# Optimization experiments

Measured on AMD Instinct MI355X. Metric: run time of the kernel, lower is better.

## Reference

```python
import jax, jax.numpy as jnp
import numpy as np

CH = 512
COND = 1280
HEADS = 8
GROUPS = CH // 8
EPS = 1e-5


def conv2d(x, w, b, pad):
    y = jax.lax.conv_general_dilated(
        x, w, window_strides=(1, 1), padding=[(pad, pad), (pad, pad)],
        dimension_numbers=('NCHW', 'OIHW', 'NCHW'))
    return y + b[None, :, None, None]


def group_norm(x, gamma, beta, groups, eps=EPS):
    b, c, h, w = x.shape
    xg = x.reshape(b, groups, c // groups, h, w)
    mu = xg.mean(axis=(2, 3, 4), keepdims=True)
    var = xg.var(axis=(2, 3, 4), keepdims=True)
    xn = ((xg - mu) * jax.lax.rsqrt(var + eps)).reshape(b, c, h, w)
    return xn * gamma[None, :, None, None] + beta[None, :, None, None]


def setup_inputs() -> dict:
    key = jax.random.key(0)
    ks = jax.random.split(key, 20)
    s = 0.05
    inp = {
        'x': jax.random.normal(ks[0], (8, CH, 32, 32), jnp.float32),
        'conditioning': jax.random.normal(ks[1], (8, COND), jnp.float32),
        # ResBlock params
        'c1w': jax.random.normal(ks[2], (CH, CH, 3, 3), jnp.float32) * s,
        'c1b': jnp.zeros((CH,), jnp.float32),
        'g1w': jnp.ones((CH,), jnp.float32),
        'g1b': jnp.zeros((CH,), jnp.float32),
        'c2w': jax.random.normal(ks[3], (CH, CH, 3, 3), jnp.float32) * s,
        'c2b': jnp.zeros((CH,), jnp.float32),
        'g2w': jnp.ones((CH,), jnp.float32),
        'g2b': jnp.zeros((CH,), jnp.float32),
        'cpw': jax.random.normal(ks[4], (CH, COND), jnp.float32) * s,
        'cpb': jnp.zeros((CH,), jnp.float32),
        'rpw': jax.random.normal(ks[5], (CH, CH, 1, 1), jnp.float32) * s,
        'rpb': jnp.zeros((CH,), jnp.float32),
        # Attention params (1x1 convs)
        'qw': jax.random.normal(ks[6], (CH, CH, 1, 1), jnp.float32) * s,
        'qb': jnp.zeros((CH,), jnp.float32),
        'kw': jax.random.normal(ks[7], (CH, CH, 1, 1), jnp.float32) * s,
        'kb': jnp.zeros((CH,), jnp.float32),
        'vw': jax.random.normal(ks[8], (CH, CH, 1, 1), jnp.float32) * s,
        'vb': jnp.zeros((CH,), jnp.float32),
        'ow': jax.random.normal(ks[9], (CH, CH, 1, 1), jnp.float32) * s,
        'ob': jnp.zeros((CH,), jnp.float32),
    }
    return inp


def reference(x, conditioning, c1w, c1b, g1w, g1b, c2w, c2b, g2w, g2b,
              cpw, cpb, rpw, rpb, qw, qb, kw, kb, vw, vb, ow, ob):
    # --- ResBlock ---
    residual = conv2d(x, rpw, rpb, 0)
    h = conv2d(x, c1w, c1b, 1)
    h = group_norm(h, g1w, g1b, GROUPS)
    h = jax.nn.silu(h)
    h = conv2d(h, c2w, c2b, 1)
    h = group_norm(h, g2w, g2b, GROUPS)
    cond = conditioning @ cpw.T + cpb  # [B, C]
    h = h * (1.0 + cond[:, :, None, None]) + residual

    # --- SpatialSelfAttention ---
    b, c, hh, ww = h.shape
    d = c // HEADS
    scale = d ** (-0.5)
    q = conv2d(h, qw, qb, 0).reshape(b, HEADS, d, hh * ww)
    k = conv2d(h, kw, kb, 0).reshape(b, HEADS, d, hh * ww)
    v = conv2d(h, vw, vb, 0).reshape(b, HEADS, d, hh * ww)
    attn = jnp.einsum('bhdn,bhdm->bhnm', q, k) * scale  # [B,H,N,N]
    attn = jax.nn.softmax(attn, axis=-1)
    out = jnp.einsum('bhnm,bhdm->bhdn', attn, v).reshape(b, c, hh, ww)
    return conv2d(out, ow, ob, 0) + h
```

## Files before the change

kernel.cpp:

```cpp
#include <hip/hip_runtime.h>
#include <hip/hip_bf16.h>

typedef unsigned short u16;
typedef __attribute__((ext_vector_type(8))) short bf8;
typedef __attribute__((ext_vector_type(4))) short bf4;
typedef __attribute__((ext_vector_type(4))) float f32x4;

#define CH_ 512
#define NSP 1024
#define NB 8
#define CONDDIM 1280
#define NGROUP 64
#define HEADS_ 8
#define HD 64
#define PR 34
#define PPB (PR*PR)
#define QSCALE 0.18033688011112042f

#define VWAIT(N) asm volatile("s_waitcnt vmcnt(" #N ")" ::: "memory")
#define SCHEDB __builtin_amdgcn_sched_barrier(0)
#define BARRIER do { SCHEDB; __builtin_amdgcn_s_barrier(); SCHEDB; } while (0)

__device__ __forceinline__ u16 f2bf(float f) {
  union { float f; unsigned u; } v; v.f = f;
  unsigned u = v.u;
  return (u16)((u + 0x7fffu + ((u >> 16) & 1u)) >> 16);
}

__device__ __forceinline__ unsigned cvt_pk_bf16(float lo, float hi) {
  unsigned r;
  asm volatile("v_cvt_pk_bf16_f32 %0, %1, %2" : "=v"(r) : "v"(lo), "v"(hi));
  return r;
}

__device__ __forceinline__ f32x4 mfma_bf16(bf8 a, bf8 b, f32x4 c) {
  return __builtin_amdgcn_mfma_f32_16x16x32_bf16(a, b, c, 0, 0, 0);
}

__device__ __forceinline__ void gload16(const void* g, void* l) {
  __builtin_amdgcn_global_load_lds((const __attribute__((address_space(1))) void*)g,
                                   (__attribute__((address_space(3))) void*)l, 16, 0, 0);
}


__global__ __launch_bounds__(1024) void pack_x_kernel(const float* __restrict__ x, u16* __restrict__ xp) {
  __shared__ float t[32][33];
  int b = blockIdx.z;
  int c0 = blockIdx.y * 32, p0 = blockIdx.x * 32;
  int tx = threadIdx.x & 31, ty = threadIdx.x >> 5;
  t[ty][tx] = x[((size_t)b * CH_ + c0 + ty) * NSP + p0 + tx];
  __syncthreads();
  int p = p0 + ty;
  int y = p >> 5, xc = p & 31;
  xp[((size_t)b * PPB + (size_t)(y + 1) * PR + xc + 1) * CH_ + c0 + tx] = f2bf(t[tx][ty]);
}

__global__ __launch_bounds__(256) void border_zero_kernel(u16* __restrict__ a, u16* __restrict__ b) {
  int id = blockIdx.x * 256 + threadIdx.x;
  if (id >= NB * 132 * 64) return;
  int ch8 = id & 63;
  int rest = id >> 6;
  int bidx = rest % 132;
  int bb = rest / 132;
  int r, c;
  if (bidx < 34)       { r = 0;          c = bidx; }
  else if (bidx < 68)  { r = 33;         c = bidx - 34; }
  else if (bidx < 100) { r = bidx - 67;  c = 0; }
  else                 { r = bidx - 99;  c = 33; }
  size_t off = ((size_t)bb * PPB + (size_t)r * PR + c) * CH_ + ch8 * 8;
  const bf8 z = {0, 0, 0, 0, 0, 0, 0, 0};
  *(bf8*)(a + off) = z;
  *(bf8*)(b + off) = z;
}

__global__ __launch_bounds__(256) void pack_w3_kernel(const float* __restrict__ w, u16* __restrict__ wp) {
  int id = blockIdx.x * 256 + threadIdx.x;
  if (id >= 9 * 64 * CH_) return;
  int co = id & (CH_ - 1);
  int cib = (id >> 9) & 63;
  int t = id >> 15;
  int dy = t / 3, dx = t % 3;
  bf8 v;
#pragma unroll
  for (int j = 0; j < 8; j++) {
    int ci = cib * 8 + j;
    v[j] = (short)f2bf(w[(((size_t)co * CH_ + ci) * 3 + dy) * 3 + dx]);
  }
  *(bf8*)(wp + ((size_t)(t * 64 + cib) * CH_ + co) * 8) = v;
}

__global__ __launch_bounds__(256) void pack_w1_kernel(const float* __restrict__ w, u16* __restrict__ wp) {
  int id = blockIdx.x * 256 + threadIdx.x;
  if (id >= 64 * CH_) return;
  int co = id & (CH_ - 1);
  int cib = id >> 9;
  bf8 v;
#pragma unroll
  for (int j = 0; j < 8; j++) v[j] = (short)f2bf(w[(size_t)co * CH_ + cib * 8 + j]);
  *(bf8*)(wp + ((size_t)cib * CH_ + co) * 8) = v;
}

__global__ __launch_bounds__(256) void cond_kernel(const float* __restrict__ cd, const float* __restrict__ cpw,
                                                   const float* __restrict__ cpb, float* __restrict__ cond) {
  int b = blockIdx.y;
  int c = blockIdx.x * 4 + (threadIdx.x >> 6);
  int lane = threadIdx.x & 63;
  const float* wrow = cpw + (size_t)c * CONDDIM;
  const float* crow = cd + (size_t)b * CONDDIM;
  float s = 0.f;
  for (int i = lane; i < CONDDIM; i += 64) s += crow[i] * wrow[i];
#pragma unroll
  for (int m = 32; m > 0; m >>= 1) s += __shfl_xor(s, m, 64);
  if (lane == 0) cond[b * CH_ + c] = s + cpb[c];
}

template <int TAPS, int PIN, int EPI>
__global__ __launch_bounds__(256, TAPS == 9 ? 4 : 3) void conv_kernel(
    const u16* __restrict__ in, const u16* __restrict__ wp, const float* __restrict__ bias,
    float* __restrict__ outf, const float* __restrict__ addf,
    u16* __restrict__ o0, u16* __restrict__ o1, u16* __restrict__ o2,
    const float* __restrict__ b0, const float* __restrict__ b1, const float* __restrict__ b2) {
  constexpr int LDSZ = (TAPS == 9) ? (2 * 14336 + 3 * 4096) : (4 * 8192 + 4 * 4096);
  __shared__ char lds[LDSZ];
  char* ldsA = lds;
  char* ldsB = lds + ((TAPS == 9) ? 2 * 14336 : 4 * 8192);

  const int b = blockIdx.z;
  int seg = 0, coy = blockIdx.y;
  if constexpr (EPI == 5) { seg = coy >> 3; coy &= 7; }
  const int co0 = coy * 64;
  const int p0 = blockIdx.x * 128;
  const int tid = threadIdx.x;
  const int lane = tid & 63, wid = tid >> 6;
  const int wv = wid >> 1, wc = wid & 1;
  const int l15 = lane & 15, lhi = lane >> 4;

  const char* aSrc;
  if constexpr (TAPS == 9) {
    aSrc = (const char*)in + ((size_t)b * PPB + (size_t)blockIdx.x * 4 * PR) * 1024;
  } else if constexpr (PIN) {
    aSrc = (const char*)in + (size_t)b * PPB * 1024;
  } else {
    aSrc = (const char*)in + ((size_t)b * NSP + p0) * 1024;
  }
  const char* bSrc = (const char*)wp + (size_t)((EPI == 5) ? seg * 524288 : 0) + co0 * 16;

  const int pB = ((tid >> 6) * 512 + (tid & 63)) * 16;
  int pA0, pA1, pA3 = 0;
  if constexpr (TAPS == 9) {
    pA0 = ((tid >> 2) << 10) + ((tid & 3) << 4);
    pA3 = ((192 + ((tid & 127) >> 2)) << 10) + ((tid & 3) << 4);
    pA1 = 0;
  } else {
    int a0 = (tid >> 2), a1 = 64 + (tid >> 2);
    if constexpr (PIN) {
      int pp0 = p0 + a0, pp1 = p0 + a1;
      int g0 = ((pp0 >> 5) + 1) * PR + (pp0 & 31) + 1;
      int g1 = ((pp1 >> 5) + 1) * PR + (pp1 & 31) + 1;
      pA0 = (g0 << 10) + ((tid & 3) << 4);
      pA1 = (g1 << 10) + ((tid & 3) << 4);
    } else {
      pA0 = (a0 << 10) + ((tid & 3) << 4);
      pA1 = (a1 << 10) + ((tid & 3) << 4);
    }
  }

  const int aAddr = (TAPS == 9) ? ((wv * 68 + l15) * 64 + lhi * 16)
                                : ((wv * 64 + l15) * 64 + lhi * 16);
  const int bAddr = (lhi * 64 + wc * 32 + l15) * 16;

  f32x4 acc[4][2];
#pragma unroll
  for (int m = 0; m < 4; m++)
#pragma unroll
    for (int n = 0; n < 2; n++) acc[m][n] = {0.f, 0.f, 0.f, 0.f};

  if constexpr (TAPS == 9) {
    gload16(aSrc + pA0,          ldsA + (wid << 10));
    gload16(aSrc + pA0 + 65536,  ldsA + 4096 + (wid << 10));
    gload16(aSrc + pA0 + 131072, ldsA + 8192 + (wid << 10));
    gload16(aSrc + pA3,          ldsA + 12288 + ((wid & 1) << 10));
    gload16(bSrc + pB,           ldsB + (wid << 10));
    gload16(bSrc + 524288 + pB,  ldsB + 4096 + (wid << 10));
    VWAIT(1);
    BARRIER;

#define PH9(KC, T, AS) do {                                                             \
    constexpr int DT = ((T) / 3) * 34 + ((T) % 3);                                      \
    const int kcn_ = ((KC) < 15) ? (KC) + 1 : 15;                                       \
    { const int kb_ = ((T) >= 7) ? kcn_ : (KC);                                         \
      constexpr int TB = ((T) + 2) % 9;                                                 \
      gload16(bSrc + (size_t)(TB * 64 + kb_ * 4) * 8192 + pB,                           \
              ldsB + (((T) + 2) % 3) * 4096 + (wid << 10)); }                           \
    if constexpr ((T) >= 4 && (T) < 7)                                                  \
      gload16(aSrc + kcn_ * 64 + pA0 + ((T) - 4) * 65536,                               \
              ldsA + (1 - (AS)) * 14336 + ((T) - 4) * 4096 + (wid << 10));              \
    if constexpr ((T) == 7)                                                             \
      gload16(aSrc + kcn_ * 64 + pA3,                                                   \
              ldsA + (1 - (AS)) * 14336 + 12288 + ((wid & 1) << 10));                   \
    SCHEDB;                                                                             \
    bf8 af0 = *(const bf8*)(ldsA + (AS) * 14336 + DT * 64 + 0    + aAddr);              \
    bf8 af1 = *(const bf8*)(ldsA + (AS) * 14336 + DT * 64 + 1024 + aAddr);              \
    bf8 af2 = *(const bf8*)(ldsA + (AS) * 14336 + DT * 64 + 2176 + aAddr);              \
    bf8 af3 = *(const bf8*)(ldsA + (AS) * 14336 + DT * 64 + 3200 + aAddr);              \
    bf8 bq0 = *(const bf8*)(ldsB + ((T) % 3) * 4096 + 0   + bAddr);                     \
    bf8 bq1 = *(const bf8*)(ldsB + ((T) % 3) * 4096 + 256 + bAddr);                     \
    __builtin_amdgcn_s_setprio(1);                                                      \
    acc[0][0] = mfma_bf16(af0, bq0, acc[0][0]);                                         \
    acc[0][1] = mfma_bf16(af0, bq1, acc[0][1]);                                         \
    acc[1][0] = mfma_bf16(af1, bq0, acc[1][0]);                                         \
    acc[1][1] = mfma_bf16(af1, bq1, acc[1][1]);                                         \
    acc[2][0] = mfma_bf16(af2, bq0, acc[2][0]);                                         \
    acc[2][1] = mfma_bf16(af2, bq1, acc[2][1]);                                         \
    acc[3][0] = mfma_bf16(af3, bq0, acc[3][0]);                                         \
    acc[3][1] = mfma_bf16(af3, bq1, acc[3][1]);                                         \
    __builtin_amdgcn_s_setprio(0);                                                      \
    if constexpr ((T) >= 4 && (T) <= 7) { VWAIT(2); } else { VWAIT(1); }                \
    BARRIER;                                                                            \
  } while (0)

    for (int kc2 = 0; kc2 < 8; kc2++) {
      PH9(kc2 * 2, 0, 0); PH9(kc2 * 2, 1, 0); PH9(kc2 * 2, 2, 0);
      PH9(kc2 * 2, 3, 0); PH9(kc2 * 2, 4, 0); PH9(kc2 * 2, 5, 0);
      PH9(kc2 * 2, 6, 0); PH9(kc2 * 2, 7, 0); PH9(kc2 * 2, 8, 0);
      PH9(kc2 * 2 + 1, 0, 1); PH9(kc2 * 2 + 1, 1, 1); PH9(kc2 * 2 + 1, 2, 1);
      PH9(kc2 * 2 + 1, 3, 1); PH9(kc2 * 2 + 1, 4, 1); PH9(kc2 * 2 + 1, 5, 1);
      PH9(kc2 * 2 + 1, 6, 1); PH9(kc2 * 2 + 1, 7, 1); PH9(kc2 * 2 + 1, 8, 1);
    }
#undef PH9
  } else {
    gload16(aSrc + pA0,         ldsA + (wid << 10));
    gload16(aSrc + pA1,         ldsA + 4096 + (wid << 10));
    gload16(bSrc + pB,          ldsB + (wid << 10));
    gload16(aSrc + 64 + pA0,    ldsA + 8192 + (wid << 10));
    gload16(aSrc + 64 + pA1,    ldsA + 8192 + 4096 + (wid << 10));
    gload16(bSrc + 32768 + pB,  ldsB + 4096 + (wid << 10));
    VWAIT(3);
    BARRIER;

#define PH1(KC, S) do {                                                                 \
    constexpr int S2 = ((S) + 2) & 3;                                                   \
    const int kcn_ = ((KC) + 2 < 16) ? (KC) + 2 : 15;                                   \
    gload16(bSrc + (size_t)kcn_ * 32768 + pB, ldsB + S2 * 4096 + (wid << 10));          \
    gload16(aSrc + kcn_ * 64 + pA0, ldsA + S2 * 8192 + (wid << 10));                    \
    gload16(aSrc + kcn_ * 64 + pA1, ldsA + S2 * 8192 + 4096 + (wid << 10));             \
    SCHEDB;                                                                             \
    bf8 af0 = *(const bf8*)(ldsA + (S) * 8192 + 0    + aAddr);                          \
    bf8 af1 = *(const bf8*)(ldsA + (S) * 8192 + 1024 + aAddr);                          \
    bf8 af2 = *(const bf8*)(ldsA + (S) * 8192 + 2048 + aAddr);                          \
    bf8 af3 = *(const bf8*)(ldsA + (S) * 8192 + 3072 + aAddr);                          \
    bf8 bq0 = *(const bf8*)(ldsB + (S) * 4096 + 0   + bAddr);                           \
    bf8 bq1 = *(const bf8*)(ldsB + (S) * 4096 + 256 + bAddr);                           \
    __builtin_amdgcn_s_setprio(1);                                                      \
    acc[0][0] = mfma_bf16(af0, bq0, acc[0][0]);                                         \
    acc[0][1] = mfma_bf16(af0, bq1, acc[0][1]);                                         \
    acc[1][0] = mfma_bf16(af1, bq0, acc[1][0]);                                         \
    acc[1][1] = mfma_bf16(af1, bq1, acc[1][1]);                                         \
    acc[2][0] = mfma_bf16(af2, bq0, acc[2][0]);                                         \
    acc[2][1] = mfma_bf16(af2, bq1, acc[2][1]);                                         \
    acc[3][0] = mfma_bf16(af3, bq0, acc[3][0]);                                         \
    acc[3][1] = mfma_bf16(af3, bq1, acc[3][1]);                                         \
    __builtin_amdgcn_s_setprio(0);                                                      \
    VWAIT(3);                                                                           \
    BARRIER;                                                                            \
  } while (0)

    for (int kc4 = 0; kc4 < 4; kc4++) {
      PH1(kc4 * 4 + 0, 0); PH1(kc4 * 4 + 1, 1); PH1(kc4 * 4 + 2, 2); PH1(kc4 * 4 + 3, 3);
    }
#undef PH1
  }

  VWAIT(0);

#pragma unroll
  for (int m = 0; m < 4; m++) {
    int pbase = p0 + wv * 64 + m * 16 + lhi * 4;
#pragma unroll
    for (int n = 0; n < 2; n++) {
      int co = co0 + wc * 32 + n * 16 + l15;
      if constexpr (EPI == 0) {
        float bv = bias[co];
#pragma unroll
        for (int r = 0; r < 4; r++)
          outf[((size_t)b * NSP + pbase + r) * CH_ + co] = acc[m][n][r] + bv;
      } else if constexpr (EPI == 2) {
        float bv = bias[co];
        f32x4 v;
#pragma unroll
        for (int r = 0; r < 4; r++)
          v[r] = acc[m][n][r] + bv + addf[((size_t)b * NSP + pbase + r) * CH_ + co];
        *(f32x4*)(outf + ((size_t)b * CH_ + co) * NSP + pbase) = v;
      } else {
        if (seg == 0) {
          float bv = b0[co];
#pragma unroll
          for (int r = 0; r < 4; r++)
            o0[((size_t)b * NSP + pbase + r) * CH_ + co] = f2bf((acc[m][n][r] + bv) * QSCALE);
        } else if (seg == 1) {
          float bv = b1[co];
#pragma unroll
          for (int r = 0; r < 4; r++)
            o1[((size_t)b * NSP + pbase + r) * CH_ + co] = f2bf(acc[m][n][r] + bv);
        } else {
          float bv = b2[co];
          union { bf4 v; unsigned long long u; } pk4;
#pragma unroll
          for (int r = 0; r < 4; r++) pk4.v[r] = (short)f2bf(acc[m][n][r] + bv);
          *(unsigned long long*)(o2 + ((size_t)b * CH_ + co) * NSP + pbase) = pk4.u;
        }
      }
    }
  }
}

template <int MODE>
__global__ __launch_bounds__(256) void gn_kernel(
    const float* __restrict__ in, const float* __restrict__ gw, const float* __restrict__ gb,
    const float* __restrict__ cond, const float* __restrict__ resid,
    float* __restrict__ outf, u16* __restrict__ outb) {
  int b = blockIdx.y, g = blockIdx.x;
  int tid = threadIdx.x;
  int c = g * 8 + (tid & 7);
  int prow = tid >> 3;
  const float* base = in + (size_t)b * NSP * CH_ + c;
  float v[32];
  float s = 0.f, ss = 0.f;
#pragma unroll
  for (int i = 0; i < 32; i++) {
    v[i] = base[(size_t)(prow + i * 32) * CH_];
    s += v[i]; ss += v[i] * v[i];
  }
  __shared__ float rs[256], rss[256];
  rs[tid] = s; rss[tid] = ss;
  __syncthreads();
  for (int off = 128; off > 0; off >>= 1) {
    if (tid < off) { rs[tid] += rs[tid + off]; rss[tid] += rss[tid + off]; }
    __syncthreads();
  }
  float mean = rs[0] * (1.f / 8192.f);
  float var = rss[0] * (1.f / 8192.f) - mean * mean;
  float inv = rsqrtf(var + 1e-5f);
  float gamma = gw[c], beta = gb[c];
  float cm = 0.f;
  if (MODE == 1) cm = 1.f + cond[b * CH_ + c];
#pragma unroll
  for (int i = 0; i < 32; i++) {
    int p = prow + i * 32;
    float y = (v[i] - mean) * inv * gamma + beta;
    if (MODE == 0) {
      float sg = 1.f / (1.f + __expf(-y));
      int yy = p >> 5, xc = p & 31;
      outb[((size_t)b * PPB + (size_t)(yy + 1) * PR + xc + 1) * CH_ + c] = f2bf(y * sg);
    } else {
      size_t idx = ((size_t)b * NSP + p) * CH_ + c;
      float z = y * cm + resid[idx];
      outf[idx] = z;
      outb[idx] = f2bf(z);
    }
  }
}

__global__ __launch_bounds__(256) void attn_kernel(const u16* __restrict__ q, const u16* __restrict__ k,
                                                   const u16* __restrict__ vT, u16* __restrict__ ao) {
  int bid = blockIdx.x;
  int swz = (bid & 7) * 64 + (bid >> 3);
  int b = swz >> 6;
  int head = (swz >> 3) & 7;
  int qt = swz & 7;
  int tid = threadIdx.x, lane = tid & 63, wid = tid >> 6;
  int l15 = lane & 15, lhi = lane >> 4;
  int cb = head * HD;
  int q0 = qt * 128 + wid * 32;

  const char* qp = (const char*)(q + (size_t)b * NSP * CH_ + cb);
  const char* kp = (const char*)(k + (size_t)b * NSP * CH_ + cb);
  const char* vp = (const char*)(vT + ((size_t)b * CH_ + cb) * NSP);

  __shared__ u16 Ksh[3][64 * 64];
  __shared__ u16 Vsh[3][64 * 64];

  bf8 aq[2][2];
#pragma unroll
  for (int qh = 0; qh < 2; qh++)
#pragma unroll
    for (int ks = 0; ks < 2; ks++)
      aq[qh][ks] = *(const bf8*)(qp + ((size_t)(q0 + qh * 16 + l15) * CH_ + ks * 32 + lhi * 8) * 2);

  f32x4 o[2][4];
  float mrow[2], lpart[2];
#pragma unroll
  for (int qh = 0; qh < 2; qh++) {
    mrow[qh] = -1e30f; lpart[qh] = 0.f;
#pragma unroll
    for (int n = 0; n < 4; n++) o[qh][n] = {0.f, 0.f, 0.f, 0.f};
  }

  auto stage = [&](int kt, int buf) {
#pragma unroll
    for (int t = 0; t < 2; t++) {
      int i = wid * 2 + t;
      int chunk = i * 64 + lane;
      int r = chunk >> 3, c = chunk & 7;
      gload16(kp + (size_t)(kt * 64 + r) * 1024 + (size_t)((c ^ (r & 7)) * 16),
              (char*)Ksh[buf] + i * 1024);
    }
#pragma unroll
    for (int t = 0; t < 2; t++) {
      int i = wid * 2 + t;
      int chunk = i * 64 + lane;
      int r = chunk >> 3, c = chunk & 7;
      gload16(vp + (size_t)r * 2048 + (size_t)(kt * 128) + (size_t)((c ^ (r & 7)) * 16),
              (char*)Vsh[buf] + i * 1024);
    }
  };

  stage(0, 0);
  stage(1, 1);

  int cB = 0, sB = 2;
  for (int kt = 0; kt < 16; ++kt) {
    if (kt < 15) { VWAIT(4); } else { VWAIT(0); }
    BARRIER;
    if (kt < 14) stage(kt + 2, sB);
    const char* Kb = (const char*)Ksh[0] + cB * 8192;
    const char* Vb = (const char*)Vsh[0] + cB * 8192;

    f32x4 sacc[2][4];
#pragma unroll
    for (int qh = 0; qh < 2; qh++)
#pragma unroll
      for (int kf = 0; kf < 4; kf++) sacc[qh][kf] = {0.f, 0.f, 0.f, 0.f};

#pragma unroll
    for (int kf = 0; kf < 4; kf++) {
      bf8 ak[2];
#pragma unroll
      for (int ks = 0; ks < 2; ks++)
        ak[ks] = *(const bf8*)(Kb + (size_t)(kf * 16 + l15) * 128 + (((ks * 4 + lhi) ^ (l15 & 7)) * 16));
#pragma unroll
      for (int qh = 0; qh < 2; qh++)
#pragma unroll
        for (int ks = 0; ks < 2; ks++)
          sacc[qh][kf] = mfma_bf16(ak[ks], aq[qh][ks], sacc[qh][kf]);
    }

    unsigned pk[2][4][2];
#pragma unroll
    for (int qh = 0; qh < 2; qh++) {
      float m0 = fmaxf(fmaxf(sacc[qh][0][0], sacc[qh][0][1]), fmaxf(sacc[qh][0][2], sacc[qh][0][3]));
      float m1 = fmaxf(fmaxf(sacc[qh][1][0], sacc[qh][1][1]), fmaxf(sacc[qh][1][2], sacc[qh][1][3]));
      float m2 = fmaxf(fmaxf(sacc[qh][2][0], sacc[qh][2][1]), fmaxf(sacc[qh][2][2], sacc[qh][2][3]));
      float m3 = fmaxf(fmaxf(sacc[qh][3][0], sacc[qh][3][1]), fmaxf(sacc[qh][3][2], sacc[qh][3][3]));
      float pml = fmaxf(fmaxf(m0, m1), fmaxf(m2, m3));
      if (__any(pml > mrow[qh] + 8.f)) {
        float pm = fmaxf(pml, __shfl_xor(pml, 16, 64));
        pm = fmaxf(pm, __shfl_xor(pm, 32, 64));
        float mn = fmaxf(mrow[qh], pm);
        float corr = exp2f(mrow[qh] - mn);
        mrow[qh] = mn;
        lpart[qh] *= corr;
        float corr_o[4];
#pragma unroll
        for (int r = 0; r < 4; r++) corr_o[r] = __shfl(corr, lhi * 4 + r, 64);
#pragma unroll
        for (int n = 0; n < 4; n++)
#pragma unroll
          for (int r = 0; r < 4; r++) o[qh][n][r] *= corr_o[r];
      }
      float rsum = 0.f;
#pragma unroll
      for (int kf = 0; kf < 4; kf++) {
        f32x4 pv;
#pragma unroll
        for (int r = 0; r < 4; r++) {
          pv[r] = exp2f(sacc[qh][kf][r] - mrow[qh]);
          rsum += pv[r];
        }
        pk[qh][kf][0] = cvt_pk_bf16(pv[0], pv[1]);
        pk[qh][kf][1] = cvt_pk_bf16(pv[2], pv[3]);
      }
      lpart[qh] += rsum;
    }

#pragma unroll
    for (int g = 0; g < 2; g++) {
      union { bf8 v8; unsigned u[4]; } ap[2];
#pragma unroll
      for (int qh = 0; qh < 2; qh++) {
        ap[qh].u[0] = pk[qh][2 * g][0];
        ap[qh].u[1] = pk[qh][2 * g][1];
        ap[qh].u[2] = pk[qh][2 * g + 1][0];
        ap[qh].u[3] = pk[qh][2 * g + 1][1];
      }
#pragma unroll
      for (int nf2 = 0; nf2 < 4; nf2++) {
        int row = nf2 * 16 + l15;
        int c0 = 4 * g + (lhi >> 1);
        union { bf8 v8; bf4 v4[2]; } bv;
        bv.v4[0] = *(const bf4*)(Vb + (size_t)row * 128 + ((c0 ^ (l15 & 7)) * 16) + (lhi & 1) * 8);
        bv.v4[1] = *(const bf4*)(Vb + (size_t)row * 128 + (((c0 + 2) ^ (l15 & 7)) * 16) + (lhi & 1) * 8);
#pragma unroll
        for (int qh = 0; qh < 2; qh++)
          o[qh][nf2] = mfma_bf16(ap[qh].v8, bv.v8, o[qh][nf2]);
      }
    }

    cB = (cB == 2) ? 0 : cB + 1;
    sB = (sB == 2) ? 0 : sB + 1;
  }

#pragma unroll
  for (int qh = 0; qh < 2; qh++) {
    float lrow = lpart[qh];
    lrow += __shfl_xor(lrow, 16, 64);
    lrow += __shfl_xor(lrow, 32, 64);
    float linv[4];
#pragma unroll
    for (int r = 0; r < 4; r++) linv[r] = 1.f / __shfl(lrow, lhi * 4 + r, 64);
#pragma unroll
    for (int nf2 = 0; nf2 < 4; nf2++)
#pragma unroll
      for (int r = 0; r < 4; r++) {
        float val = o[qh][nf2][r] * linv[r];
        ao[((size_t)b * NSP + q0 + qh * 16 + lhi * 4 + r) * CH_ + cb + nf2 * 16 + l15] = f2bf(val);
      }
  }
}


extern "C" void kernel_launch(void* const* d_in, const int* in_sizes, int n_in,
                              void* d_out, int out_size, void* d_ws, size_t ws_size,
                              hipStream_t stream) {
  const float* x    = (const float*)d_in[0];
  const float* cnd  = (const float*)d_in[1];
  const float* c1w  = (const float*)d_in[2];
  const float* c1b  = (const float*)d_in[3];
  const float* g1w  = (const float*)d_in[4];
  const float* g1b  = (const float*)d_in[5];
  const float* c2w  = (const float*)d_in[6];
  const float* c2b  = (const float*)d_in[7];
  const float* g2w  = (const float*)d_in[8];
  const float* g2b  = (const float*)d_in[9];
  const float* cpw  = (const float*)d_in[10];
  const float* cpb  = (const float*)d_in[11];
  const float* rpw  = (const float*)d_in[12];
  const float* rpb  = (const float*)d_in[13];
  const float* qw   = (const float*)d_in[14];
  const float* qb   = (const float*)d_in[15];
  const float* kw   = (const float*)d_in[16];
  const float* kb   = (const float*)d_in[17];
  const float* vw   = (const float*)d_in[18];
  const float* vb   = (const float*)d_in[19];
  const float* ow   = (const float*)d_in[20];
  const float* ob   = (const float*)d_in[21];
  float* out = (float*)d_out;

  char* ws = (char*)d_ws;
  size_t off = 0;
  auto alloc = [&](size_t bytes) -> char* {
    char* p = ws + off;
    off = (off + bytes + 255) & ~(size_t)255;
    return p;
  };
  const size_t ACT_F = (size_t)NB * NSP * CH_ * 4;
  const size_t ACT_B = (size_t)NB * NSP * CH_ * 2;
  const size_t PAD_B = (size_t)NB * PPB * CH_ * 2;

  u16* xp    = (u16*)alloc(PAD_B);
  u16* h1p   = (u16*)alloc(PAD_B);
  u16* w1p   = (u16*)alloc((size_t)9 * CH_ * CH_ * 2);
  u16* w2p   = (u16*)alloc((size_t)9 * CH_ * CH_ * 2);
  u16* wrp   = (u16*)alloc((size_t)CH_ * CH_ * 2);
  u16* wqkv  = (u16*)alloc((size_t)3 * CH_ * CH_ * 2);
  u16* wop   = (u16*)alloc((size_t)CH_ * CH_ * 2);
  float* cndv = (float*)alloc((size_t)NB * CH_ * 4);
  float* resid = (float*)alloc(ACT_F);
  float* h12  = (float*)alloc(ACT_F);
  u16* hb    = (u16*)alloc(ACT_B);
  u16* qbuf  = (u16*)alloc(ACT_B);
  u16* kbuf  = (u16*)alloc(ACT_B);
  u16* vTb   = (u16*)alloc(ACT_B);
  u16* aob   = (u16*)alloc(ACT_B);
  if (off > ws_size) return;

  dim3 tgrid(NSP / 32, CH_ / 32, NB);
  border_zero_kernel<<<(NB * 132 * 64 + 255) / 256, 256, 0, stream>>>(xp, h1p);
  pack_x_kernel<<<tgrid, 1024, 0, stream>>>(x, xp);
  pack_w3_kernel<<<(9 * 64 * CH_ + 255) / 256, 256, 0, stream>>>(c1w, w1p);
  pack_w3_kernel<<<(9 * 64 * CH_ + 255) / 256, 256, 0, stream>>>(c2w, w2p);
  pack_w1_kernel<<<(64 * CH_) / 256, 256, 0, stream>>>(rpw, wrp);
  pack_w1_kernel<<<(64 * CH_) / 256, 256, 0, stream>>>(qw, wqkv);
  pack_w1_kernel<<<(64 * CH_) / 256, 256, 0, stream>>>(kw, wqkv + (size_t)CH_ * CH_);
  pack_w1_kernel<<<(64 * CH_) / 256, 256, 0, stream>>>(vw, wqkv + (size_t)2 * CH_ * CH_);
  pack_w1_kernel<<<(64 * CH_) / 256, 256, 0, stream>>>(ow, wop);
  cond_kernel<<<dim3(CH_ / 4, NB), 256, 0, stream>>>(cnd, cpw, cpb, cndv);

  dim3 ggrid(NSP / 128, CH_ / 64, NB);
  dim3 qgrid(NSP / 128, 3 * CH_ / 64, NB);
  conv_kernel<9, 1, 0><<<ggrid, 256, 0, stream>>>(xp, w1p, c1b, h12, nullptr,
                                                  nullptr, nullptr, nullptr, nullptr, nullptr, nullptr);
  conv_kernel<1, 1, 0><<<ggrid, 256, 0, stream>>>(xp, wrp, rpb, resid, nullptr,
                                                  nullptr, nullptr, nullptr, nullptr, nullptr, nullptr);
  gn_kernel<0><<<dim3(NGROUP, NB), 256, 0, stream>>>(h12, g1w, g1b, nullptr, nullptr, nullptr, h1p);
  conv_kernel<9, 1, 0><<<ggrid, 256, 0, stream>>>(h1p, w2p, c2b, h12, nullptr,
                                                  nullptr, nullptr, nullptr, nullptr, nullptr, nullptr);
  gn_kernel<1><<<dim3(NGROUP, NB), 256, 0, stream>>>(h12, g2w, g2b, cndv, resid, h12, hb);
  conv_kernel<1, 0, 5><<<qgrid, 256, 0, stream>>>(hb, wqkv, nullptr, nullptr, nullptr,
                                                  qbuf, kbuf, vTb, qb, kb, vb);
  attn_kernel<<<512, 256, 0, stream>>>(qbuf, kbuf, vTb, aob);
  conv_kernel<1, 0, 2><<<ggrid, 256, 0, stream>>>(aob, wop, ob, out, h12,
                                                  nullptr, nullptr, nullptr, nullptr, nullptr, nullptr);
}
```

Baseline: 265.2 us.

## Split attention keys in two with combine pass, batch weight packing launches

The attention kernel now splits the key sequence into two halves (split-K flash attention), doubling the block count to 1024. Each block writes partial normalized outputs plus row sums and maxima, and a new combine kernel merges them. V is stored in a permuted column order so each lane reads one 16-byte vector instead of two 8-byte pieces. The seven weight-packing launches are merged into two using a grid y dimension. The split adds an extra kernel and partial-output traffic, reuses the resid and h1p buffers as scratch, and reduces pipelining from triple to double buffering.

```diff
diff --git a/kernel.cpp b/kernel.cpp
--- a/kernel.cpp
+++ b/kernel.cpp
@@ -2,6 +2,7 @@
 #include <hip/hip_bf16.h>
 
 typedef unsigned short u16;
+typedef unsigned long long u64;
 typedef __attribute__((ext_vector_type(8))) short bf8;
 typedef __attribute__((ext_vector_type(4))) short bf4;
 typedef __attribute__((ext_vector_type(4))) float f32x4;
@@ -25,6 +26,10 @@
   union { float f; unsigned u; } v; v.f = f;
   unsigned u = v.u;
   return (u16)((u + 0x7fffu + ((u >> 16) & 1u)) >> 16);
+}
+
+__device__ __forceinline__ float b2f(u16 x) {
+  union { unsigned u; float f; } v; v.u = ((unsigned)x) << 16; return v.f;
 }
 
 __device__ __forceinline__ unsigned cvt_pk_bf16(float lo, float hi) {
@@ -73,9 +78,12 @@
   *(bf8*)(b + off) = z;
 }
 
-__global__ __launch_bounds__(256) void pack_w3_kernel(const float* __restrict__ w, u16* __restrict__ wp) {
+__global__ __launch_bounds__(256) void pack_w3_kernel(const float* __restrict__ wA, const float* __restrict__ wB,
+                                                      u16* __restrict__ dA, u16* __restrict__ dB) {
   int id = blockIdx.x * 256 + threadIdx.x;
   if (id >= 9 * 64 * CH_) return;
+  const float* w = blockIdx.y ? wB : wA;
+  u16* wp = blockIdx.y ? dB : dA;
   int co = id & (CH_ - 1);
   int cib = (id >> 9) & 63;
   int t = id >> 15;
@@ -89,9 +97,21 @@
   *(bf8*)(wp + ((size_t)(t * 64 + cib) * CH_ + co) * 8) = v;
 }
 
-__global__ __launch_bounds__(256) void pack_w1_kernel(const float* __restrict__ w, u16* __restrict__ wp) {
+__global__ __launch_bounds__(256) void pack_w1_kernel(
+    const float* __restrict__ s0, const float* __restrict__ s1, const float* __restrict__ s2,
+    const float* __restrict__ s3, const float* __restrict__ s4,
+    u16* __restrict__ d0, u16* __restrict__ d1, u16* __restrict__ d2,
+    u16* __restrict__ d3, u16* __restrict__ d4) {
   int id = blockIdx.x * 256 + threadIdx.x;
   if (id >= 64 * CH_) return;
+  const float* w; u16* wp;
+  switch (blockIdx.y) {
+    case 0: w = s0; wp = d0; break;
+    case 1: w = s1; wp = d1; break;
+    case 2: w = s2; wp = d2; break;
+    case 3: w = s3; wp = d3; break;
+    default: w = s4; wp = d4; break;
+  }
   int co = id & (CH_ - 1);
   int cib = id >> 9;
   bf8 v;
@@ -304,10 +324,11 @@
             o1[((size_t)b * NSP + pbase + r) * CH_ + co] = f2bf(acc[m][n][r] + bv);
         } else {
           float bv = b2[co];
-          union { bf4 v; unsigned long long u; } pk4;
+          union { bf4 v; u64 u; } pk4;
 #pragma unroll
           for (int r = 0; r < 4; r++) pk4.v[r] = (short)f2bf(acc[m][n][r] + bv);
-          *(unsigned long long*)(o2 + ((size_t)b * CH_ + co) * NSP + pbase) = pk4.u;
+          int np = (pbase & ~31) | ((pbase & 12) << 1) | ((pbase & 16) >> 2);
+          *(u64*)(o2 + ((size_t)b * CH_ + co) * NSP + np) = pk4.u;
         }
       }
     }
@@ -362,23 +383,25 @@
 }
 
 __global__ __launch_bounds__(256) void attn_kernel(const u16* __restrict__ q, const u16* __restrict__ k,
-                                                   const u16* __restrict__ vT, u16* __restrict__ ao) {
+                                                   const u16* __restrict__ vT, u16* __restrict__ opart,
+                                                   float* __restrict__ lbuf, float* __restrict__ mbuf) {
   int bid = blockIdx.x;
-  int swz = (bid & 7) * 64 + (bid >> 3);
-  int b = swz >> 6;
-  int head = (swz >> 3) & 7;
-  int qt = swz & 7;
+  int swz = (bid & 7) * 128 + (bid >> 3);
+  int b = swz >> 7;
+  int head = (swz >> 4) & 7;
+  int qt = (swz >> 1) & 7;
+  int s = swz & 1;
   int tid = threadIdx.x, lane = tid & 63, wid = tid >> 6;
   int l15 = lane & 15, lhi = lane >> 4;
   int cb = head * HD;
   int q0 = qt * 128 + wid * 32;
 
   const char* qp = (const char*)(q + (size_t)b * NSP * CH_ + cb);
-  const char* kp = (const char*)(k + (size_t)b * NSP * CH_ + cb);
-  const char* vp = (const char*)(vT + ((size_t)b * CH_ + cb) * NSP);
-
-  __shared__ u16 Ksh[3][64 * 64];
-  __shared__ u16 Vsh[3][64 * 64];
+  const char* kp = (const char*)(k + (size_t)b * NSP * CH_ + cb) + (size_t)s * 512 * 1024;
+  const char* vp = (const char*)(vT + ((size_t)b * CH_ + cb) * NSP) + s * 1024;
+
+  __shared__ u16 Ksh[2][64 * 64];
+  __shared__ u16 Vsh[2][64 * 64];
 
   bf8 aq[2][2];
 #pragma unroll
@@ -416,15 +439,12 @@
   };
 
   stage(0, 0);
-  stage(1, 1);
-
-  int cB = 0, sB = 2;
-  for (int kt = 0; kt < 16; ++kt) {
-    if (kt < 15) { VWAIT(4); } else { VWAIT(0); }
-    BARRIER;
-    if (kt < 14) stage(kt + 2, sB);
-    const char* Kb = (const char*)Ksh[0] + cB * 8192;
-    const char* Vb = (const char*)Vsh[0] + cB * 8192;
+
+  for (int kt = 0; kt < 8; ++kt) {
+    __syncthreads();
+    if (kt < 7) stage(kt + 1, (kt + 1) & 1);
+    const char* Kb = (const char*)Ksh[kt & 1];
+    const char* Vb = (const char*)Vsh[kt & 1];
 
     f32x4 sacc[2][4];
 #pragma unroll
@@ -496,18 +516,12 @@
 #pragma unroll
       for (int nf2 = 0; nf2 < 4; nf2++) {
         int row = nf2 * 16 + l15;
-        int c0 = 4 * g + (lhi >> 1);
-        union { bf8 v8; bf4 v4[2]; } bv;
-        bv.v4[0] = *(const bf4*)(Vb + (size_t)row * 128 + ((c0 ^ (l15 & 7)) * 16) + (lhi & 1) * 8);
-        bv.v4[1] = *(const bf4*)(Vb + (size_t)row * 128 + (((c0 + 2) ^ (l15 & 7)) * 16) + (lhi & 1) * 8);
+        bf8 bv8 = *(const bf8*)(Vb + (size_t)row * 128 + (((4 * g + lhi) ^ (l15 & 7)) * 16));
 #pragma unroll
         for (int qh = 0; qh < 2; qh++)
-          o[qh][nf2] = mfma_bf16(ap[qh].v8, bv.v8, o[qh][nf2]);
+          o[qh][nf2] = mfma_bf16(ap[qh].v8, bv8, o[qh][nf2]);
       }
     }
-
-    cB = (cB == 2) ? 0 : cB + 1;
-    sB = (sB == 2) ? 0 : sB + 1;
   }
 
 #pragma unroll
@@ -515,6 +529,12 @@
     float lrow = lpart[qh];
     lrow += __shfl_xor(lrow, 16, 64);
     lrow += __shfl_xor(lrow, 32, 64);
+    if (lhi == 0) {
+      int qq = q0 + qh * 16 + l15;
+      int li = ((s * NB + b) * 8 + head) * 1024 + qq;
+      lbuf[li] = lrow;
+      mbuf[li] = mrow[qh];
+    }
     float linv[4];
 #pragma unroll
     for (int r = 0; r < 4; r++) linv[r] = 1.f / __shfl(lrow, lhi * 4 + r, 64);
@@ -523,9 +543,35 @@
 #pragma unroll
       for (int r = 0; r < 4; r++) {
         float val = o[qh][nf2][r] * linv[r];
-        ao[((size_t)b * NSP + q0 + qh * 16 + lhi * 4 + r) * CH_ + cb + nf2 * 16 + l15] = f2bf(val);
+        opart[((size_t)(s * NB + b) * NSP + q0 + qh * 16 + lhi * 4 + r) * CH_ + cb + nf2 * 16 + l15] = f2bf(val);
       }
   }
+}
+
+__global__ __launch_bounds__(256) void combine_kernel(
+    const u16* __restrict__ opart, const float* __restrict__ lbuf, const float* __restrict__ mbuf,
+    u16* __restrict__ ao) {
+  int id = blockIdx.x * 256 + threadIdx.x;
+  int c8 = id & 63;
+  int n = (id >> 6) & 1023;
+  int b = id >> 16;
+  int head = c8 >> 3;
+  int i1 = (b * 8 + head) * 1024 + n;
+  int i2 = ((NB + b) * 8 + head) * 1024 + n;
+  float l1 = lbuf[i1], l2 = lbuf[i2];
+  float m1 = mbuf[i1], m2 = mbuf[i2];
+  float m = fmaxf(m1, m2);
+  float w1 = l1 * exp2f(m1 - m), w2 = l2 * exp2f(m2 - m);
+  float inv = 1.f / (w1 + w2);
+  w1 *= inv; w2 *= inv;
+  size_t base = ((size_t)b * NSP + n) * CH_ + c8 * 8;
+  bf8 v1 = *(const bf8*)(opart + base);
+  bf8 v2 = *(const bf8*)(opart + (size_t)NB * NSP * CH_ + base);
+  bf8 out;
+#pragma unroll
+  for (int j = 0; j < 8; j++)
+    out[j] = (short)f2bf(w1 * b2f((u16)v1[j]) + w2 * b2f((u16)v2[j]));
+  *(bf8*)(ao + base) = out;
 }
 
 
@@ -584,16 +630,17 @@
   u16* aob   = (u16*)alloc(ACT_B);
   if (off > ws_size) return;
 
+  u16* opart = (u16*)resid;
+  float* lbuf = (float*)h1p;
+  float* mbuf = (float*)((char*)h1p + (1 << 19));
+
   dim3 tgrid(NSP / 32, CH_ / 32, NB);
   border_zero_kernel<<<(NB * 132 * 64 + 255) / 256, 256, 0, stream>>>(xp, h1p);
   pack_x_kernel<<<tgrid, 1024, 0, stream>>>(x, xp);
-  pack_w3_kernel<<<(9 * 64 * CH_ + 255) / 256, 256, 0, stream>>>(c1w, w1p);
-  pack_w3_kernel<<<(9 * 64 * CH_ + 255) / 256, 256, 0, stream>>>(c2w, w2p);
-  pack_w1_kernel<<<(64 * CH_) / 256, 256, 0, stream>>>(rpw, wrp);
-  pack_w1_kernel<<<(64 * CH_) / 256, 256, 0, stream>>>(qw, wqkv);
-  pack_w1_kernel<<<(64 * CH_) / 256, 256, 0, stream>>>(kw, wqkv + (size_t)CH_ * CH_);
-  pack_w1_kernel<<<(64 * CH_) / 256, 256, 0, stream>>>(vw, wqkv + (size_t)2 * CH_ * CH_);
-  pack_w1_kernel<<<(64 * CH_) / 256, 256, 0, stream>>>(ow, wop);
+  pack_w3_kernel<<<dim3((9 * 64 * CH_ + 255) / 256, 2), 256, 0, stream>>>(c1w, c2w, w1p, w2p);
+  pack_w1_kernel<<<dim3((64 * CH_) / 256, 5), 256, 0, stream>>>(
+      rpw, qw, kw, vw, ow,
+      wrp, wqkv, wqkv + (size_t)CH_ * CH_, wqkv + (size_t)2 * CH_ * CH_, wop);
   cond_kernel<<<dim3(CH_ / 4, NB), 256, 0, stream>>>(cnd, cpw, cpb, cndv);
 
   dim3 ggrid(NSP / 128, CH_ / 64, NB);
@@ -608,7 +655,8 @@
   gn_kernel<1><<<dim3(NGROUP, NB), 256, 0, stream>>>(h12, g2w, g2b, cndv, resid, h12, hb);
   conv_kernel<1, 0, 5><<<qgrid, 256, 0, stream>>>(hb, wqkv, nullptr, nullptr, nullptr,
                                                   qbuf, kbuf, vTb, qb, kb, vb);
-  attn_kernel<<<512, 256, 0, stream>>>(qbuf, kbuf, vTb, aob);
+  attn_kernel<<<1024, 256, 0, stream>>>(qbuf, kbuf, vTb, opart, lbuf, mbuf);
+  combine_kernel<<<2048, 256, 0, stream>>>(opart, lbuf, mbuf, aob);
   conv_kernel<1, 0, 2><<<ggrid, 256, 0, stream>>>(aob, wop, ob, out, h12,
                                                   nullptr, nullptr, nullptr, nullptr, nullptr, nullptr);
 }
```

Measured after the change: 263.4 us. No clear change (-0.7%).
